# Kernel optimization log

Measured on AMD Instinct MI355X. Metric: run time of the kernel, lower is better.

The kernel has to match this reference:

```python
import jax, jax.numpy as jnp
import numpy as np

D_MODEL = 512
D_INNER = 1024   # expand=2
D_STATE = 16
D_CONV = 4
DT_RANK = 32     # ceil(d_model/16)
B, L = 2, 2048


def _params(kbase):
    kk = jax.random.split(kbase, 9)
    n = lambda k, s, sc: jax.random.normal(k, s, jnp.float32) * sc
    return dict(
        Win=n(kk[0], (2 * D_INNER, D_MODEL), D_MODEL ** -0.5),
        convw=n(kk[1], (D_INNER, 1, D_CONV), 0.2),
        convb=n(kk[2], (D_INNER,), 0.02),
        Wx=n(kk[3], (DT_RANK + 2 * D_STATE, D_INNER), D_INNER ** -0.5),
        Wdt=n(kk[4], (D_INNER, DT_RANK), DT_RANK ** -0.5),
        dtb=n(kk[5], (D_INNER,), 0.1),
        Alog=n(kk[6], (D_INNER, D_STATE), 0.5),
        Dp=n(kk[7], (D_INNER,), 1.0),
        Wout=n(kk[8], (D_MODEL, D_INNER), D_INNER ** -0.5),
    )


def setup_inputs() -> dict:
    key = jax.random.key(0)
    k0, kf, kr = jax.random.split(key, 3)
    inp = {"hidden_states": jax.random.normal(k0, (B, L, D_MODEL), jnp.float32)}
    for name, v in _params(kf).items():
        inp[name + "_f"] = v
    for name, v in _params(kr).items():
        inp[name + "_r"] = v
    return inp


def _mamba(x, Win, convw, convb, Wx, Wdt, dtb, Alog, Dp, Wout):
    # x: (B, L, D_MODEL)
    Bb = x.shape[0]
    xz = jnp.einsum('bld,ed->ble', x, Win)            # (B, L, 2*D_INNER)
    xs, z = jnp.split(xz, 2, axis=-1)
    # causal depthwise conv over length
    xc = jnp.swapaxes(xs, 1, 2)                       # (B, D_INNER, L)
    xc = jax.lax.conv_general_dilated(
        xc, convw, (1,), [(D_CONV - 1, 0)], feature_group_count=D_INNER)
    xs = jax.nn.silu(jnp.swapaxes(xc + convb[None, :, None], 1, 2))  # (B, L, D_INNER)
    # input-dependent SSM params
    x_dbl = jnp.einsum('bld,ed->ble', xs, Wx)         # (B, L, DT_RANK+2*D_STATE)
    dt = x_dbl[..., :DT_RANK]
    Bm = x_dbl[..., DT_RANK:DT_RANK + D_STATE]        # (B, L, D_STATE)
    Cm = x_dbl[..., DT_RANK + D_STATE:]               # (B, L, D_STATE)
    dt = jax.nn.softplus(jnp.einsum('blr,dr->bld', dt, Wdt) + dtb)   # (B, L, D_INNER)
    A = -jnp.exp(Alog)                                # (D_INNER, D_STATE), strictly negative
    dA = jnp.exp(dt[..., None] * A)                   # (B, L, D_INNER, D_STATE)
    dBu = dt[..., None] * Bm[:, :, None, :] * xs[..., None]

    def step(h, inp):
        dA_t, dBu_t, C_t = inp
        h = dA_t * h + dBu_t                          # (B, D_INNER, D_STATE)
        return h, jnp.einsum('bds,bs->bd', h, C_t)

    h0 = jnp.zeros((Bb, D_INNER, D_STATE), x.dtype)
    _, ys = jax.lax.scan(
        step, h0,
        (jnp.moveaxis(dA, 1, 0), jnp.moveaxis(dBu, 1, 0), jnp.moveaxis(Cm, 1, 0)))
    y = jnp.moveaxis(ys, 0, 1) + xs * Dp              # (B, L, D_INNER)
    y = y * jax.nn.silu(z)                            # gated output
    return jnp.einsum('bld,ed->ble', y, Wout)         # (B, L, D_MODEL)


def reference(hidden_states,
              Win_f, convw_f, convb_f, Wx_f, Wdt_f, dtb_f, Alog_f, Dp_f, Wout_f,
              Win_r, convw_r, convb_r, Wx_r, Wdt_r, dtb_r, Alog_r, Dp_r, Wout_r):
    out_f = _mamba(hidden_states, Win_f, convw_f, convb_f, Wx_f, Wdt_f, dtb_f,
                   Alog_f, Dp_f, Wout_f)
    out_r = _mamba(hidden_states[:, ::-1, :], Win_r, convw_r, convb_r, Wx_r,
                   Wdt_r, dtb_r, Alog_r, Dp_r, Wout_r)[:, ::-1, :]
    return out_f + out_r  # bidirectional_strategy == 'add'
```

## Files before the change

kernel.cpp:

```cpp
#include <hip/hip_runtime.h>
#include <cmath>

#define B_   2
#define L_   2048
#define DM_  512
#define DI_  1024
#define DS_  16
#define DTR_ 32
#define M_   (B_*L_)
#define NC_  64
#define CL_  32
#define KS_  8
#define LOG2E_ 1.44269504088896340736f
#define LN2_   0.69314718055994530942f

typedef __attribute__((ext_vector_type(8))) short short8;
typedef __attribute__((ext_vector_type(4))) float floatx4;

__device__ inline unsigned short f2bf(float f) {
  unsigned u = __float_as_uint(f);
  unsigned r = (u + 0x7fffu + ((u >> 16) & 1u)) >> 16;
  return (unsigned short)r;
}
__device__ inline float bf2f(unsigned short u) {
  return __uint_as_float(((unsigned)u) << 16);
}
__device__ inline unsigned short f2h(float f) {
  _Float16 h = (_Float16)f;
  return *(unsigned short*)&h;
}
__device__ inline float h2f(unsigned short u) {
  _Float16 h = *(_Float16*)&u;
  return (float)h;
}
__device__ inline float fexp2(float x) { return __builtin_amdgcn_exp2f(x); }
__device__ inline float flog2(float x) { return __builtin_amdgcn_logf(x); }

__device__ inline void gload_lds16(const unsigned short* g, unsigned short* l) {
  __builtin_amdgcn_global_load_lds(
      (const __attribute__((address_space(1))) void*)g,
      (__attribute__((address_space(3))) void*)l, 16, 0, 0);
}

__global__ __launch_bounds__(256, 2) void gemm1_mfma_k(
    const unsigned short* __restrict__ A,
    const unsigned short* __restrict__ Wf, const unsigned short* __restrict__ Wr,
    unsigned short* __restrict__ Cf, unsigned short* __restrict__ Cr,
    int N, int K)
{
  __shared__ unsigned short At[2][128 * 32];
  __shared__ unsigned short Wtf[2][128 * 32];
  __shared__ unsigned short Wtr[2][128 * 32];
  const int tid  = threadIdx.x;
  const int w    = tid >> 6;
  const int lane = tid & 63;
  const int wm   = w >> 1, wn = w & 1;
  const int row0 = blockIdx.y * 128, col0 = blockIdx.x * 128;
  const int lrow  = lane >> 2;
  const int lkoff = (lane & 3) * 8;
  const int fr = lane & 15;
  const int fq = (lane >> 4) * 8;

  floatx4 accf[4][4], accr[4][4];
#pragma unroll
  for (int i = 0; i < 4; ++i)
#pragma unroll
    for (int j = 0; j < 4; ++j)
#pragma unroll
      for (int r = 0; r < 4; ++r) { accf[i][j][r] = 0.f; accr[i][j][r] = 0.f; }

  auto stage = [&](int buf, int k0) {
#pragma unroll
    for (int j = 0; j < 2; ++j) {
      int r = w * 32 + j * 16;
      gload_lds16(A  + (size_t)(row0 + r + lrow) * K + k0 + lkoff, At[buf]  + r * 32);
      gload_lds16(Wf + (size_t)(col0 + r + lrow) * K + k0 + lkoff, Wtf[buf] + r * 32);
      gload_lds16(Wr + (size_t)(col0 + r + lrow) * K + k0 + lkoff, Wtr[buf] + r * 32);
    }
  };
  auto compute = [&](int buf) {
    short8 af[4], bff[4], bfr[4];
#pragma unroll
    for (int i = 0; i < 4; ++i) {
      af[i]  = *(const short8*)&At[buf][(64 * wm + 16 * i + fr) * 32 + fq];
      bff[i] = *(const short8*)&Wtf[buf][(64 * wn + 16 * i + fr) * 32 + fq];
      bfr[i] = *(const short8*)&Wtr[buf][(64 * wn + 16 * i + fr) * 32 + fq];
    }
#pragma unroll
    for (int i = 0; i < 4; ++i)
#pragma unroll
      for (int j = 0; j < 4; ++j) {
        accf[i][j] = __builtin_amdgcn_mfma_f32_16x16x32_bf16(af[i], bff[j], accf[i][j], 0, 0, 0);
        accr[i][j] = __builtin_amdgcn_mfma_f32_16x16x32_bf16(af[i], bfr[j], accr[i][j], 0, 0, 0);
      }
  };

  const int NT = K >> 5;
  stage(0, 0);
  __syncthreads();
  int cur = 0;
  for (int t = 0; t < NT - 1; ++t) {
    stage(cur ^ 1, (t + 1) << 5);
    compute(cur);
    __syncthreads();
    cur ^= 1;
  }
  compute(cur);

#pragma unroll
  for (int i = 0; i < 4; ++i) {
    int rg = row0 + 64 * wm + 16 * i + ((lane >> 4) << 2);
#pragma unroll
    for (int j = 0; j < 4; ++j) {
      int cg = col0 + 64 * wn + 16 * j + (lane & 15);
#pragma unroll
      for (int r = 0; r < 4; ++r) {
        Cf[(size_t)(rg + r) * N + cg] = f2bf(accf[i][j][r]);
        Cr[(size_t)(rg + r) * N + cg] = f2bf(accr[i][j][r]);
      }
    }
  }
}

__global__ __launch_bounds__(256) void gemm4_fused_k(
    const unsigned short* __restrict__ ybf, const unsigned short* __restrict__ Woutbf,
    const unsigned short* __restrict__ ybr, const unsigned short* __restrict__ Woutbr,
    float* __restrict__ out)
{
  __shared__ unsigned short At[2][2][64 * 32];
  __shared__ unsigned short Wt[2][2][64 * 32];
  const int tid  = threadIdx.x;
  const int w    = tid >> 6;
  const int lane = tid & 63;
  const int col0 = blockIdx.x * 64;
  const int row0 = blockIdx.y * 64;
  const int lrow  = lane >> 2;
  const int lkoff = (lane & 3) * 8;
  const int fr = lane & 15;
  const int fq = (lane >> 4) * 8;

  floatx4 acc[4];
#pragma unroll
  for (int j = 0; j < 4; ++j)
#pragma unroll
    for (int r = 0; r < 4; ++r) acc[j][r] = 0.f;

  auto stage = [&](int buf, int t) {
    const unsigned short* A = (t & 16) ? ybr : ybf;
    const unsigned short* W = (t & 16) ? Woutbr : Woutbf;
    const int k0 = (t & 15) << 6;
#pragma unroll
    for (int h = 0; h < 2; ++h) {
      gload_lds16(A + (size_t)(row0 + 16 * w + lrow) * DI_ + k0 + 32 * h + lkoff,
                  At[buf][h] + (16 * w) * 32);
      gload_lds16(W + (size_t)(col0 + 16 * w + lrow) * DI_ + k0 + 32 * h + lkoff,
                  Wt[buf][h] + (16 * w) * 32);
    }
  };
  auto compute = [&](int buf) {
    short8 af[2], bf[2][4];
#pragma unroll
    for (int h = 0; h < 2; ++h) {
      af[h] = *(const short8*)&At[buf][h][(16 * w + fr) * 32 + fq];
#pragma unroll
      for (int j = 0; j < 4; ++j)
        bf[h][j] = *(const short8*)&Wt[buf][h][(16 * j + fr) * 32 + fq];
    }
#pragma unroll
    for (int h = 0; h < 2; ++h)
#pragma unroll
      for (int j = 0; j < 4; ++j)
        acc[j] = __builtin_amdgcn_mfma_f32_16x16x32_bf16(af[h], bf[h][j], acc[j], 0, 0, 0);
  };

  stage(0, 0);
  __syncthreads();
  int cur = 0;
  for (int t = 0; t < 31; ++t) {
    stage(cur ^ 1, t + 1);
    compute(cur);
    __syncthreads();
    cur ^= 1;
  }
  compute(cur);

  const int rg = row0 + 16 * w + ((lane >> 4) << 2);
#pragma unroll
  for (int j = 0; j < 4; ++j) {
    int cg = col0 + 16 * j + (lane & 15);
#pragma unroll
    for (int r = 0; r < 4; ++r)
      out[(size_t)(rg + r) * DM_ + cg] = acc[j][r];
  }
}

__global__ __launch_bounds__(256) void gemm2_mfma_k(
    const unsigned short* __restrict__ xsbf, const unsigned short* __restrict__ xsbr,
    const unsigned short* __restrict__ Wxbf, const unsigned short* __restrict__ Wxbr,
    float* __restrict__ part)
{
  __shared__ unsigned short At[2][128 * 32];
  __shared__ unsigned short Wt[2][64 * 32];
  const int tid  = threadIdx.x;
  const int w    = tid >> 6;
  const int lane = tid & 63;
  const int ks   = blockIdx.x;
  const int row0 = blockIdx.y * 128;
  const int dir  = blockIdx.z;
  const unsigned short* A = dir ? xsbr : xsbf;
  const unsigned short* W = dir ? Wxbr : Wxbf;
  const int kbase = ks * (DI_ / KS_);
  const int lrow  = lane >> 2;
  const int lkoff = (lane & 3) * 8;
  const int fr = lane & 15;
  const int fq = (lane >> 4) * 8;

  floatx4 acc[2][4];
#pragma unroll
  for (int i = 0; i < 2; ++i)
#pragma unroll
    for (int j = 0; j < 4; ++j)
#pragma unroll
      for (int r = 0; r < 4; ++r) acc[i][j][r] = 0.f;

  auto stage = [&](int buf, int k0) {
#pragma unroll
    for (int j = 0; j < 2; ++j) {
      int r = w * 32 + j * 16;
      gload_lds16(A + (size_t)(row0 + r + lrow) * DI_ + kbase + k0 + lkoff, At[buf] + r * 32);
    }
    int r = w * 16;
    gload_lds16(W + (size_t)(r + lrow) * DI_ + kbase + k0 + lkoff, Wt[buf] + r * 32);
  };
  auto compute = [&](int buf) {
    short8 af[2], bf[4];
#pragma unroll
    for (int i = 0; i < 2; ++i)
      af[i] = *(const short8*)&At[buf][(32 * w + 16 * i + fr) * 32 + fq];
#pragma unroll
    for (int j = 0; j < 4; ++j)
      bf[j] = *(const short8*)&Wt[buf][(16 * j + fr) * 32 + fq];
#pragma unroll
    for (int i = 0; i < 2; ++i)
#pragma unroll
      for (int j = 0; j < 4; ++j)
        acc[i][j] = __builtin_amdgcn_mfma_f32_16x16x32_bf16(af[i], bf[j], acc[i][j], 0, 0, 0);
  };

  const int NT = (DI_ / KS_) >> 5;
  stage(0, 0);
  __syncthreads();
  int cur = 0;
  for (int t = 0; t < NT - 1; ++t) {
    stage(cur ^ 1, (t + 1) << 5);
    compute(cur);
    __syncthreads();
    cur ^= 1;
  }
  compute(cur);

  float* dst = part + (((size_t)dir * KS_ + ks) * M_) * 64;
#pragma unroll
  for (int i = 0; i < 2; ++i) {
    int rg = row0 + 32 * w + 16 * i + ((lane >> 4) << 2);
#pragma unroll
    for (int j = 0; j < 4; ++j) {
      int cg = 16 * j + (lane & 15);
#pragma unroll
      for (int r = 0; r < 4; ++r)
        dst[(size_t)(rg + r) * 64 + cg] = acc[i][j][r];
    }
  }
}

__global__ __launch_bounds__(256) void reduce_part_k(
    const float* __restrict__ part, float* __restrict__ xdf, float* __restrict__ xdr,
    unsigned short* __restrict__ drbf, unsigned short* __restrict__ drbr)
{
  int g = blockIdx.x * 256 + threadIdx.x;
  int n4  = g & 15;
  int m   = (g >> 4) & (M_ - 1);
  int dir = g >> 16;
  const float* p = part + ((size_t)dir * KS_ * M_ + m) * 64 + n4 * 4;
  float4 s = make_float4(0.f, 0.f, 0.f, 0.f);
#pragma unroll
  for (int ks = 0; ks < KS_; ++ks) {
    float4 v = *(const float4*)(p + (size_t)ks * M_ * 64);
    s.x += v.x; s.y += v.y; s.z += v.z; s.w += v.w;
  }
  float* xd = dir ? xdr : xdf;
  *(float4*)(xd + (size_t)m * 64 + n4 * 4) = s;
  if (n4 < 8) {
    unsigned short* dr = dir ? drbr : drbf;
    ushort4 o;
    o.x = f2bf(s.x); o.y = f2bf(s.y); o.z = f2bf(s.z); o.w = f2bf(s.w);
    *(ushort4*)(dr + (size_t)m * 32 + n4 * 4) = o;
  }
}

struct CastArgs {
  const float* src[9];
  unsigned short* dst[9];
  int start[9];
  int n[9];
};

__global__ __launch_bounds__(256) void cast_multi_k(
    CastArgs a, int total4,
    const float* __restrict__ Alf, const float* __restrict__ Alr,
    float* __restrict__ Atf, float* __restrict__ Atr)
{
  int g = blockIdx.x * 256 + threadIdx.x;
  if (g >= total4) return;
  if (g < 8192) {
    const float* Al = (g < 4096) ? Alf : Alr;
    float* At = (g < 4096) ? Atf : Atr;
    int off = (g & 4095) * 4;
    float4 v = *(const float4*)(Al + off);
    float4 o = make_float4(-__expf(v.x) * LOG2E_, -__expf(v.y) * LOG2E_,
                           -__expf(v.z) * LOG2E_, -__expf(v.w) * LOG2E_);
    *(float4*)(At + off) = o;
  }
  int e = g * 4;
#pragma unroll 1
  for (int s = 0; s < 9; ++s) {
    if (e < a.start[s] + a.n[s]) {
      int off = e - a.start[s];
      float4 v = *(const float4*)(a.src[s] + off);
      ushort4 o;
      o.x = f2bf(v.x); o.y = f2bf(v.y); o.z = f2bf(v.z); o.w = f2bf(v.w);
      *(ushort4*)(a.dst[s] + off) = o;
      return;
    }
  }
}

__global__ __launch_bounds__(256) void gemm3_mfma_k(
    const unsigned short* __restrict__ drbf, const unsigned short* __restrict__ drbr,
    const unsigned short* __restrict__ Wdtbf, const unsigned short* __restrict__ Wdtbr,
    const float* __restrict__ b0, const float* __restrict__ b1,
    unsigned short* __restrict__ C0, unsigned short* __restrict__ C1)
{
  __shared__ unsigned short At[128 * 32];
  __shared__ unsigned short Wt[128 * 32];
  const unsigned short* A = blockIdx.z ? drbr : drbf;
  const unsigned short* W = blockIdx.z ? Wdtbr : Wdtbf;
  const float* bias = blockIdx.z ? b1 : b0;
  unsigned short* C = blockIdx.z ? C1 : C0;
  const int tid  = threadIdx.x;
  const int w    = tid >> 6;
  const int lane = tid & 63;
  const int wm   = w >> 1, wn = w & 1;
  const int row0 = blockIdx.y * 128, col0 = blockIdx.x * 128;
  const int lrow  = lane >> 2;
  const int lkoff = (lane & 3) * 8;
  const int fr = lane & 15;
  const int fq = (lane >> 4) * 8;

#pragma unroll
  for (int j = 0; j < 2; ++j) {
    int r = w * 32 + j * 16;
    gload_lds16(A + (size_t)(row0 + r + lrow) * DTR_ + lkoff, At + r * 32);
    gload_lds16(W + (size_t)(col0 + r + lrow) * DTR_ + lkoff, Wt + r * 32);
  }
  __syncthreads();
  short8 af[4], bf[4];
#pragma unroll
  for (int i = 0; i < 4; ++i) {
    af[i] = *(const short8*)&At[(64 * wm + 16 * i + fr) * 32 + fq];
    bf[i] = *(const short8*)&Wt[(64 * wn + 16 * i + fr) * 32 + fq];
  }
  floatx4 acc[4][4];
#pragma unroll
  for (int i = 0; i < 4; ++i)
#pragma unroll
    for (int j = 0; j < 4; ++j) {
#pragma unroll
      for (int r = 0; r < 4; ++r) acc[i][j][r] = 0.f;
      acc[i][j] = __builtin_amdgcn_mfma_f32_16x16x32_bf16(af[i], bf[j], acc[i][j], 0, 0, 0);
    }
#pragma unroll
  for (int i = 0; i < 4; ++i) {
    int rg = row0 + 64 * wm + 16 * i + ((lane >> 4) << 2);
#pragma unroll
    for (int j = 0; j < 4; ++j) {
      int cg = col0 + 64 * wn + 16 * j + (lane & 15);
      float bv = bias[cg];
#pragma unroll
      for (int r = 0; r < 4; ++r) {
        float v = acc[i][j][r] + bv;
        float e = fexp2(-fabsf(v) * LOG2E_);
        float sp = fmaxf(v, 0.f) + LN2_ * flog2(1.f + e);
        C[(size_t)(rg + r) * DI_ + cg] = f2h(sp);
      }
    }
  }
}

__global__ __launch_bounds__(256) void conv_silu_k(
    const unsigned short* __restrict__ xzbf, const unsigned short* __restrict__ xzbr,
    const float* __restrict__ cwf, const float* __restrict__ cbf,
    const float* __restrict__ cwr, const float* __restrict__ cbr,
    unsigned short* __restrict__ xsbf, unsigned short* __restrict__ xsbr)
{
  int bid = blockIdx.x;
  int t2  = bid & (L_ / 2 - 1);
  int b   = (bid >> 10) & (B_ - 1);
  int dir = bid >> 11;
  int t   = t2 << 1;
  const unsigned short* xz = dir ? xzbr : xzbf;
  const float* cw = dir ? cwr : cwf;
  const float* cb = dir ? cbr : cbf;
  unsigned short* xsb = dir ? xsbr : xsbf;
  int d0 = threadIdx.x << 2;
  float wv[4][4];
#pragma unroll
  for (int i = 0; i < 4; ++i) {
    float4 w4 = *(const float4*)(cw + (size_t)(d0 + i) * 4);
    wv[i][0] = w4.x; wv[i][1] = w4.y; wv[i][2] = w4.z; wv[i][3] = w4.w;
  }
  float4 cbv = *(const float4*)(cb + d0);
  float accA[4] = {cbv.x, cbv.y, cbv.z, cbv.w};
  float accB[4] = {cbv.x, cbv.y, cbv.z, cbv.w};
#pragma unroll
  for (int j = 0; j < 5; ++j) {
    int tt = dir ? (t + 4 - j) : (t - 3 + j);
    if (tt >= 0 && tt < L_) {
      ushort4 v = *(const ushort4*)(xz + ((size_t)b * L_ + tt) * 2048 + d0);
      float f0 = bf2f(v.x), f1 = bf2f(v.y), f2 = bf2f(v.z), f3 = bf2f(v.w);
      if (j < 4) {
        accA[0] = fmaf(wv[0][j], f0, accA[0]);
        accA[1] = fmaf(wv[1][j], f1, accA[1]);
        accA[2] = fmaf(wv[2][j], f2, accA[2]);
        accA[3] = fmaf(wv[3][j], f3, accA[3]);
      }
      if (j >= 1) {
        accB[0] = fmaf(wv[0][j - 1], f0, accB[0]);
        accB[1] = fmaf(wv[1][j - 1], f1, accB[1]);
        accB[2] = fmaf(wv[2][j - 1], f2, accB[2]);
        accB[3] = fmaf(wv[3][j - 1], f3, accB[3]);
      }
    }
  }
  int tA = dir ? t + 1 : t;
  int tB = dir ? t : t + 1;
  ushort4 oa, ob;
#pragma unroll
  for (int i = 0; i < 4; ++i) {
    float sa = accA[i] * __builtin_amdgcn_rcpf(1.f + fexp2(-accA[i] * LOG2E_));
    float sb = accB[i] * __builtin_amdgcn_rcpf(1.f + fexp2(-accB[i] * LOG2E_));
    ((unsigned short*)&oa)[i] = f2bf(sa);
    ((unsigned short*)&ob)[i] = f2bf(sb);
  }
  *(ushort4*)(xsb + ((size_t)b * L_ + tA) * DI_ + d0) = oa;
  *(ushort4*)(xsb + ((size_t)b * L_ + tB) * DI_ + d0) = ob;
}

__global__ __launch_bounds__(256) void scan_passA_k(
    const unsigned short* __restrict__ dtf, const unsigned short* __restrict__ dtr,
    const unsigned short* __restrict__ xsbf, const unsigned short* __restrict__ xsbr,
    const float* __restrict__ xdf, const float* __restrict__ xdr,
    const float* __restrict__ Atabf, const float* __restrict__ Atabr,
    float* __restrict__ E, float* __restrict__ dts)
{
  __shared__ float bS[CL_][16];
  int bid  = blockIdx.x;
  int dgrp = bid & 3;
  int c    = (bid >> 2) & (NC_ - 1);
  int b    = (bid >> 8) & 1;
  int dir  = bid >> 9;
  int d    = (dgrp << 8) + threadIdx.x;
  const unsigned short* dt = dir ? dtr : dtf;
  const unsigned short* xs = dir ? xsbr : xsbf;
  const float* xd = dir ? xdr : xdf;
  const float* At = dir ? Atabr : Atabf;
  if (threadIdx.x < CL_ * 4) {
    int li = threadIdx.x >> 2;
    int lc = threadIdx.x & 3;
    *(float4*)&bS[li][lc * 4] =
        *(const float4*)(xd + ((size_t)b * L_ + c * CL_ + li) * 64 + 32 + lc * 4);
  }
  float Ai2[16];
#pragma unroll
  for (int q = 0; q < 4; ++q) {
    float4 a4 = *(const float4*)(At + (size_t)d * 16 + q * 4);
    Ai2[4*q] = a4.x; Ai2[4*q+1] = a4.y; Ai2[4*q+2] = a4.z; Ai2[4*q+3] = a4.w;
  }
  float h[16];
#pragma unroll
  for (int s = 0; s < 16; ++s) h[s] = 0.f;
  int t0 = c * CL_ + (dir ? CL_ - 1 : 0);
  const long sdt = (dir ? -1L : 1L) * DI_;
  const unsigned short* dtp = dt + ((size_t)b * L_ + t0) * DI_ + d;
  const unsigned short* xsp = xs + ((size_t)b * L_ + t0) * DI_ + d;
  float dtsum = 0.f;
  __syncthreads();
#pragma unroll 2
  for (int i = 0; i < CL_; ++i) {
    int row = dir ? (CL_ - 1 - i) : i;
    float dtv = h2f(*dtp);
    float xv  = bf2f(*xsp);
    float Bv[16];
#pragma unroll
    for (int q = 0; q < 4; ++q) {
      float4 bq = *(const float4*)&bS[row][4 * q];
      Bv[4*q] = bq.x; Bv[4*q+1] = bq.y; Bv[4*q+2] = bq.z; Bv[4*q+3] = bq.w;
    }
    float dtx = dtv * xv;
    dtsum += dtv;
#pragma unroll
    for (int s = 0; s < 16; ++s) {
      float dA = fexp2(dtv * Ai2[s]);
      h[s] = fmaf(dA, h[s], dtx * Bv[s]);
    }
    dtp += sdt; xsp += sdt;
  }
  size_t base = ((((size_t)dir * B_ + b) * NC_ + c) * DI_ + d) * 16;
#pragma unroll
  for (int q = 0; q < 4; ++q)
    *(float4*)(E + base + q * 4) = make_float4(h[4*q], h[4*q+1], h[4*q+2], h[4*q+3]);
  dts[(((size_t)dir * B_ + b) * NC_ + c) * DI_ + d] = dtsum;
}

__global__ __launch_bounds__(256) void scan_prefix_k(
    const float* __restrict__ E, const float* __restrict__ dts,
    const float* __restrict__ Atabf, const float* __restrict__ Atabr,
    float* __restrict__ Hin)
{
  int gid = blockIdx.x * 256 + threadIdx.x;
  int s   = gid & 15;
  int d   = (gid >> 4) & (DI_ - 1);
  int b   = (gid >> 14) & 1;
  int dir = gid >> 15;
  float Ai2 = (dir ? Atabr : Atabf)[(size_t)d * 16 + s];
  size_t eb  = (((size_t)dir * B_ + b) * NC_) * DI_ * 16 + (size_t)d * 16 + s;
  size_t db2 = (((size_t)dir * B_ + b) * NC_) * DI_ + d;
  const long es = (long)DI_ * 16;
  float h = 0.f;
  if (!dir) {
    size_t idx = eb;
    size_t di  = db2;
    float Ec = E[idx], dc = dts[di];
#pragma unroll 2
    for (int c = 0; c < NC_ - 1; ++c) {
      float En = E[idx + es];
      float dn = dts[di + DI_];
      Hin[idx] = h;
      h = fmaf(fexp2(dc * Ai2), h, Ec);
      Ec = En; dc = dn; idx += es; di += DI_;
    }
    Hin[idx] = h;
  } else {
    size_t idx = eb + (size_t)(NC_ - 1) * es;
    size_t di  = db2 + (size_t)(NC_ - 1) * DI_;
    float Ec = E[idx], dc = dts[di];
#pragma unroll 2
    for (int c = 0; c < NC_ - 1; ++c) {
      float En = E[idx - es];
      float dn = dts[di - DI_];
      Hin[idx] = h;
      h = fmaf(fexp2(dc * Ai2), h, Ec);
      Ec = En; dc = dn; idx -= es; di -= DI_;
    }
    Hin[idx] = h;
  }
}

__global__ __launch_bounds__(256) void scan_passC_k(
    const unsigned short* __restrict__ dtf, const unsigned short* __restrict__ dtr,
    const unsigned short* __restrict__ xsbf, const unsigned short* __restrict__ xsbr,
    const float* __restrict__ xdf, const float* __restrict__ xdr,
    const unsigned short* __restrict__ xzbf, const unsigned short* __restrict__ xzbr,
    const float* __restrict__ Atabf, const float* __restrict__ Atabr,
    const float* __restrict__ Dpf, const float* __restrict__ Dpr,
    const float* __restrict__ Hin,
    unsigned short* __restrict__ ybf, unsigned short* __restrict__ ybr)
{
  __shared__ float bcS[CL_][32];
  int bid  = blockIdx.x;
  int dgrp = bid & 3;
  int c    = (bid >> 2) & (NC_ - 1);
  int b    = (bid >> 8) & 1;
  int dir  = bid >> 9;
  int d    = (dgrp << 8) + threadIdx.x;
  const unsigned short* dt  = dir ? dtr : dtf;
  const unsigned short* xs = dir ? xsbr : xsbf;
  const float* xd  = dir ? xdr : xdf;
  const unsigned short* xz = dir ? xzbr : xzbf;
  const float* At  = dir ? Atabr : Atabf;
  unsigned short* yb = dir ? ybr : ybf;
  float Dpv = (dir ? Dpr : Dpf)[d];
  {
    int li = threadIdx.x >> 3;
    int lc = threadIdx.x & 7;
    *(float4*)&bcS[li][lc * 4] =
        *(const float4*)(xd + ((size_t)b * L_ + c * CL_ + li) * 64 + 32 + lc * 4);
  }
  float Ai2[16];
#pragma unroll
  for (int q = 0; q < 4; ++q) {
    float4 a4 = *(const float4*)(At + (size_t)d * 16 + q * 4);
    Ai2[4*q] = a4.x; Ai2[4*q+1] = a4.y; Ai2[4*q+2] = a4.z; Ai2[4*q+3] = a4.w;
  }
  size_t hb = ((((size_t)dir * B_ + b) * NC_ + c) * DI_ + d) * 16;
  float h[16];
#pragma unroll
  for (int q = 0; q < 4; ++q) {
    float4 hv = *(const float4*)(Hin + hb + q * 4);
    h[4*q] = hv.x; h[4*q+1] = hv.y; h[4*q+2] = hv.z; h[4*q+3] = hv.w;
  }
  int t0 = c * CL_ + (dir ? CL_ - 1 : 0);
  const long sdt = (dir ? -1L : 1L) * DI_;
  const long sz_ = (dir ? -1L : 1L) * 2048;
  const unsigned short* dtp = dt + ((size_t)b * L_ + t0) * DI_ + d;
  const unsigned short* xsp = xs + ((size_t)b * L_ + t0) * DI_ + d;
  const unsigned short* zp = xz + ((size_t)b * L_ + t0) * 2048 + DI_ + d;
  unsigned short* ybp = yb + ((size_t)b * L_ + t0) * DI_ + d;
  __syncthreads();
#pragma unroll 2
  for (int i = 0; i < CL_; ++i) {
    int row = dir ? (CL_ - 1 - i) : i;
    float dtv = h2f(*dtp);
    float xv  = bf2f(*xsp);
    float z   = bf2f(*zp);
    float Bv[16], Cv[16];
#pragma unroll
    for (int q = 0; q < 4; ++q) {
      float4 bq = *(const float4*)&bcS[row][4 * q];
      float4 cq = *(const float4*)&bcS[row][16 + 4 * q];
      Bv[4*q] = bq.x; Bv[4*q+1] = bq.y; Bv[4*q+2] = bq.z; Bv[4*q+3] = bq.w;
      Cv[4*q] = cq.x; Cv[4*q+1] = cq.y; Cv[4*q+2] = cq.z; Cv[4*q+3] = cq.w;
    }
    float dtx = dtv * xv;
    float yacc = 0.f;
#pragma unroll
    for (int s = 0; s < 16; ++s) {
      float dA = fexp2(dtv * Ai2[s]);
      h[s] = fmaf(dA, h[s], dtx * Bv[s]);
      yacc = fmaf(h[s], Cv[s], yacc);
    }
    float yv = fmaf(xv, Dpv, yacc);
    float sz = z * __builtin_amdgcn_rcpf(1.f + fexp2(-z * LOG2E_));
    *ybp = f2bf(yv * sz);
    dtp += sdt; xsp += sdt; zp += sz_; ybp += sdt;
  }
}

extern "C" void kernel_launch(void* const* d_in, const int* in_sizes, int n_in,
                              void* d_out, int out_size, void* d_ws, size_t ws_size,
                              hipStream_t stream)
{
  const float* x       = (const float*)d_in[0];
  const float* Win_f   = (const float*)d_in[1];
  const float* convw_f = (const float*)d_in[2];
  const float* convb_f = (const float*)d_in[3];
  const float* Wx_f    = (const float*)d_in[4];
  const float* Wdt_f   = (const float*)d_in[5];
  const float* dtb_f   = (const float*)d_in[6];
  const float* Alog_f  = (const float*)d_in[7];
  const float* Dp_f    = (const float*)d_in[8];
  const float* Wout_f  = (const float*)d_in[9];
  const float* Win_r   = (const float*)d_in[10];
  const float* convw_r = (const float*)d_in[11];
  const float* convb_r = (const float*)d_in[12];
  const float* Wx_r    = (const float*)d_in[13];
  const float* Wdt_r   = (const float*)d_in[14];
  const float* dtb_r   = (const float*)d_in[15];
  const float* Alog_r  = (const float*)d_in[16];
  const float* Dp_r    = (const float*)d_in[17];
  const float* Wout_r  = (const float*)d_in[18];
  float* out = (float*)d_out;

  float* ws  = (float*)d_ws;
  float* xdf = ws;
  float* xdr = xdf + (size_t)M_ * 64;
  unsigned short* dtf = (unsigned short*)(xdr + (size_t)M_ * 64);
  unsigned short* dtr = dtf + (size_t)M_ * DI_;
  float* Eb  = (float*)(dtr + (size_t)M_ * DI_);
  float* Hb  = Eb + (size_t)2 * B_ * NC_ * DI_ * 16;
  float* dtsb = Hb + (size_t)2 * B_ * NC_ * DI_ * 16;
  float* part2 = Eb;
  unsigned short* xzbf    = (unsigned short*)(dtsb + (size_t)2 * B_ * NC_ * DI_);
  unsigned short* xzbr    = xzbf + (size_t)M_ * 2048;
  unsigned short* xb      = xzbr + (size_t)M_ * 2048;
  unsigned short* Winb_f  = xb + (size_t)M_ * DM_;
  unsigned short* Winb_r  = Winb_f + (size_t)2048 * DM_;
  unsigned short* Woutb_f = Winb_r + (size_t)2048 * DM_;
  unsigned short* Woutb_r = Woutb_f + (size_t)DM_ * DI_;
  unsigned short* ybf     = Woutb_r + (size_t)DM_ * DI_;
  unsigned short* ybr     = ybf + (size_t)M_ * DI_;
  unsigned short* xsbf    = ybr + (size_t)M_ * DI_;
  unsigned short* xsbr    = xsbf + (size_t)M_ * DI_;
  unsigned short* Wxb_f   = xsbr + (size_t)M_ * DI_;
  unsigned short* Wxb_r   = Wxb_f + (size_t)64 * DI_;
  unsigned short* Wdtb_f  = Wxb_r + (size_t)64 * DI_;
  unsigned short* Wdtb_r  = Wdtb_f + (size_t)DI_ * DTR_;
  unsigned short* drbf    = Wdtb_r + (size_t)DI_ * DTR_;
  unsigned short* drbr    = drbf + (size_t)M_ * DTR_;
  float* Atabf = (float*)(drbr + (size_t)M_ * DTR_);
  float* Atabr = Atabf + (size_t)DI_ * DS_;

  dim3 blk(256);

  {
    CastArgs ca;
    ca.src[0] = x;      ca.dst[0] = xb;      ca.n[0] = M_ * DM_;
    ca.src[1] = Win_f;  ca.dst[1] = Winb_f;  ca.n[1] = 2048 * DM_;
    ca.src[2] = Win_r;  ca.dst[2] = Winb_r;  ca.n[2] = 2048 * DM_;
    ca.src[3] = Wout_f; ca.dst[3] = Woutb_f; ca.n[3] = DM_ * DI_;
    ca.src[4] = Wout_r; ca.dst[4] = Woutb_r; ca.n[4] = DM_ * DI_;
    ca.src[5] = Wx_f;   ca.dst[5] = Wxb_f;   ca.n[5] = 64 * DI_;
    ca.src[6] = Wx_r;   ca.dst[6] = Wxb_r;   ca.n[6] = 64 * DI_;
    ca.src[7] = Wdt_f;  ca.dst[7] = Wdtb_f;  ca.n[7] = DI_ * DTR_;
    ca.src[8] = Wdt_r;  ca.dst[8] = Wdtb_r;  ca.n[8] = DI_ * DTR_;
    int st = 0;
    for (int s = 0; s < 9; ++s) { ca.start[s] = st; st += ca.n[s]; }
    int total4 = st / 4;
    cast_multi_k<<<(total4 + 255) / 256, blk, 0, stream>>>(
        ca, total4, Alog_f, Alog_r, Atabf, Atabr);
  }

  gemm1_mfma_k<<<dim3(2048 / 128, M_ / 128), blk, 0, stream>>>(
      xb, Winb_f, Winb_r, xzbf, xzbr, 2048, DM_);

  conv_silu_k<<<2 * B_ * (L_ / 2), blk, 0, stream>>>(xzbf, xzbr, convw_f, convb_f,
      convw_r, convb_r, xsbf, xsbr);

  gemm2_mfma_k<<<dim3(KS_, M_ / 128, 2), blk, 0, stream>>>(
      xsbf, xsbr, Wxb_f, Wxb_r, part2);
  reduce_part_k<<<(2 * M_ * 16) / 256, blk, 0, stream>>>(part2, xdf, xdr,
      drbf, drbr);

  gemm3_mfma_k<<<dim3(DI_ / 128, M_ / 128, 2), blk, 0, stream>>>(
      drbf, drbr, Wdtb_f, Wdtb_r, dtb_f, dtb_r, dtf, dtr);

  scan_passA_k<<<2 * B_ * NC_ * 4, blk, 0, stream>>>(dtf, dtr, xsbf, xsbr,
      xdf, xdr, Atabf, Atabr, Eb, dtsb);
  scan_prefix_k<<<(2 * B_ * DI_ * 16) / 256, blk, 0, stream>>>(
      Eb, dtsb, Atabf, Atabr, Hb);
  scan_passC_k<<<2 * B_ * NC_ * 4, blk, 0, stream>>>(dtf, dtr, xsbf, xsbr,
      xdf, xdr, xzbf, xzbr, Atabf, Atabr, Dp_f, Dp_r, Hb, ybf, ybr);

  gemm4_fused_k<<<dim3(DM_ / 64, M_ / 64), blk, 0, stream>>>(
      ybf, Woutb_f, ybr, Woutb_r, out);
}
```

Measured before the change: 261.0 us.

## Store chunk scan states in fp16, batch prefix loads, widen conv outputs per block

The chunk-end states E and the chunk-entry states Hin move from fp32 to fp16 storage, which halves the traffic between pass A, the prefix scan and pass C. The prefix scan now preloads eight chunks of E and dts before running the serial recurrence, so more loads are in flight. The conv+SiLU kernel computes four timesteps per thread instead of two, reusing the overlapping input rows and launching half as many blocks. The cost is fp16 rounding of the carried scan states, which could lose precision or overflow if states grow large.

```diff
diff --git a/kernel.cpp b/kernel.cpp
--- a/kernel.cpp
+++ b/kernel.cpp
@@ -404,10 +404,10 @@
     unsigned short* __restrict__ xsbf, unsigned short* __restrict__ xsbr)
 {
   int bid = blockIdx.x;
-  int t2  = bid & (L_ / 2 - 1);
-  int b   = (bid >> 10) & (B_ - 1);
-  int dir = bid >> 11;
-  int t   = t2 << 1;
+  int tg  = bid & (L_ / 4 - 1);
+  int b   = (bid >> 9) & (B_ - 1);
+  int dir = bid >> 10;
+  int t   = tg << 2;
   const unsigned short* xz = dir ? xzbr : xzbf;
   const float* cw = dir ? cwr : cwf;
   const float* cb = dir ? cbr : cbf;
@@ -420,40 +420,39 @@
     wv[i][0] = w4.x; wv[i][1] = w4.y; wv[i][2] = w4.z; wv[i][3] = w4.w;
   }
   float4 cbv = *(const float4*)(cb + d0);
-  float accA[4] = {cbv.x, cbv.y, cbv.z, cbv.w};
-  float accB[4] = {cbv.x, cbv.y, cbv.z, cbv.w};
-#pragma unroll
-  for (int j = 0; j < 5; ++j) {
-    int tt = dir ? (t + 4 - j) : (t - 3 + j);
+  float acc[4][4];
+#pragma unroll
+  for (int k = 0; k < 4; ++k) {
+    acc[k][0] = cbv.x; acc[k][1] = cbv.y; acc[k][2] = cbv.z; acc[k][3] = cbv.w;
+  }
+#pragma unroll
+  for (int m = 0; m < 7; ++m) {
+    int tt = dir ? (t + 6 - m) : (t - 3 + m);
     if (tt >= 0 && tt < L_) {
       ushort4 v = *(const ushort4*)(xz + ((size_t)b * L_ + tt) * 2048 + d0);
       float f0 = bf2f(v.x), f1 = bf2f(v.y), f2 = bf2f(v.z), f3 = bf2f(v.w);
-      if (j < 4) {
-        accA[0] = fmaf(wv[0][j], f0, accA[0]);
-        accA[1] = fmaf(wv[1][j], f1, accA[1]);
-        accA[2] = fmaf(wv[2][j], f2, accA[2]);
-        accA[3] = fmaf(wv[3][j], f3, accA[3]);
+#pragma unroll
+      for (int k = 0; k < 4; ++k) {
+        int j = dir ? (m - 3 + k) : (m - k);
+        if (j >= 0 && j < 4) {
+          acc[k][0] = fmaf(wv[0][j], f0, acc[k][0]);
+          acc[k][1] = fmaf(wv[1][j], f1, acc[k][1]);
+          acc[k][2] = fmaf(wv[2][j], f2, acc[k][2]);
+          acc[k][3] = fmaf(wv[3][j], f3, acc[k][3]);
+        }
       }
-      if (j >= 1) {
-        accB[0] = fmaf(wv[0][j - 1], f0, accB[0]);
-        accB[1] = fmaf(wv[1][j - 1], f1, accB[1]);
-        accB[2] = fmaf(wv[2][j - 1], f2, accB[2]);
-        accB[3] = fmaf(wv[3][j - 1], f3, accB[3]);
-      }
-    }
-  }
-  int tA = dir ? t + 1 : t;
-  int tB = dir ? t : t + 1;
-  ushort4 oa, ob;
-#pragma unroll
-  for (int i = 0; i < 4; ++i) {
-    float sa = accA[i] * __builtin_amdgcn_rcpf(1.f + fexp2(-accA[i] * LOG2E_));
-    float sb = accB[i] * __builtin_amdgcn_rcpf(1.f + fexp2(-accB[i] * LOG2E_));
-    ((unsigned short*)&oa)[i] = f2bf(sa);
-    ((unsigned short*)&ob)[i] = f2bf(sb);
-  }
-  *(ushort4*)(xsb + ((size_t)b * L_ + tA) * DI_ + d0) = oa;
-  *(ushort4*)(xsb + ((size_t)b * L_ + tB) * DI_ + d0) = ob;
+    }
+  }
+#pragma unroll
+  for (int k = 0; k < 4; ++k) {
+    ushort4 o;
+#pragma unroll
+    for (int i = 0; i < 4; ++i) {
+      float s = acc[k][i] * __builtin_amdgcn_rcpf(1.f + fexp2(-acc[k][i] * LOG2E_));
+      ((unsigned short*)&o)[i] = f2bf(s);
+    }
+    *(ushort4*)(xsb + ((size_t)b * L_ + (t + k)) * DI_ + d0) = o;
+  }
 }
 
 __global__ __launch_bounds__(256) void scan_passA_k(
@@ -461,7 +460,7 @@
     const unsigned short* __restrict__ xsbf, const unsigned short* __restrict__ xsbr,
     const float* __restrict__ xdf, const float* __restrict__ xdr,
     const float* __restrict__ Atabf, const float* __restrict__ Atabr,
-    float* __restrict__ E, float* __restrict__ dts)
+    unsigned short* __restrict__ E, float* __restrict__ dts)
 {
   __shared__ float bS[CL_][16];
   int bid  = blockIdx.x;
@@ -516,16 +515,19 @@
     dtp += sdt; xsp += sdt;
   }
   size_t base = ((((size_t)dir * B_ + b) * NC_ + c) * DI_ + d) * 16;
-#pragma unroll
-  for (int q = 0; q < 4; ++q)
-    *(float4*)(E + base + q * 4) = make_float4(h[4*q], h[4*q+1], h[4*q+2], h[4*q+3]);
+  unsigned pk[8];
+#pragma unroll
+  for (int q = 0; q < 8; ++q)
+    pk[q] = (unsigned)f2h(h[2*q]) | ((unsigned)f2h(h[2*q+1]) << 16);
+  *(uint4*)(E + base)     = make_uint4(pk[0], pk[1], pk[2], pk[3]);
+  *(uint4*)(E + base + 8) = make_uint4(pk[4], pk[5], pk[6], pk[7]);
   dts[(((size_t)dir * B_ + b) * NC_ + c) * DI_ + d] = dtsum;
 }
 
 __global__ __launch_bounds__(256) void scan_prefix_k(
-    const float* __restrict__ E, const float* __restrict__ dts,
+    const unsigned short* __restrict__ E, const float* __restrict__ dts,
     const float* __restrict__ Atabf, const float* __restrict__ Atabr,
-    float* __restrict__ Hin)
+    unsigned short* __restrict__ Hin)
 {
   int gid = blockIdx.x * 256 + threadIdx.x;
   int s   = gid & 15;
@@ -535,34 +537,44 @@
   float Ai2 = (dir ? Atabr : Atabf)[(size_t)d * 16 + s];
   size_t eb  = (((size_t)dir * B_ + b) * NC_) * DI_ * 16 + (size_t)d * 16 + s;
   size_t db2 = (((size_t)dir * B_ + b) * NC_) * DI_ + d;
-  const long es = (long)DI_ * 16;
+  const size_t es = (size_t)DI_ * 16;
   float h = 0.f;
   if (!dir) {
     size_t idx = eb;
     size_t di  = db2;
-    float Ec = E[idx], dc = dts[di];
-#pragma unroll 2
-    for (int c = 0; c < NC_ - 1; ++c) {
-      float En = E[idx + es];
-      float dn = dts[di + DI_];
-      Hin[idx] = h;
-      h = fmaf(fexp2(dc * Ai2), h, Ec);
-      Ec = En; dc = dn; idx += es; di += DI_;
-    }
-    Hin[idx] = h;
+#pragma unroll 1
+    for (int cb = 0; cb < NC_; cb += 8) {
+      unsigned short Ev[8]; float dv[8];
+#pragma unroll
+      for (int k = 0; k < 8; ++k) {
+        Ev[k] = E[idx + (size_t)k * es];
+        dv[k] = dts[di + (size_t)k * DI_];
+      }
+#pragma unroll
+      for (int k = 0; k < 8; ++k) {
+        Hin[idx + (size_t)k * es] = f2h(h);
+        h = fmaf(fexp2(dv[k] * Ai2), h, h2f(Ev[k]));
+      }
+      idx += 8 * es; di += 8 * (size_t)DI_;
+    }
   } else {
     size_t idx = eb + (size_t)(NC_ - 1) * es;
     size_t di  = db2 + (size_t)(NC_ - 1) * DI_;
-    float Ec = E[idx], dc = dts[di];
-#pragma unroll 2
-    for (int c = 0; c < NC_ - 1; ++c) {
-      float En = E[idx - es];
-      float dn = dts[di - DI_];
-      Hin[idx] = h;
-      h = fmaf(fexp2(dc * Ai2), h, Ec);
-      Ec = En; dc = dn; idx -= es; di -= DI_;
-    }
-    Hin[idx] = h;
+#pragma unroll 1
+    for (int cb = 0; cb < NC_; cb += 8) {
+      unsigned short Ev[8]; float dv[8];
+#pragma unroll
+      for (int k = 0; k < 8; ++k) {
+        Ev[k] = E[idx - (size_t)k * es];
+        dv[k] = dts[di - (size_t)k * DI_];
+      }
+#pragma unroll
+      for (int k = 0; k < 8; ++k) {
+        Hin[idx - (size_t)k * es] = f2h(h);
+        h = fmaf(fexp2(dv[k] * Ai2), h, h2f(Ev[k]));
+      }
+      idx -= 8 * es; di -= 8 * (size_t)DI_;
+    }
   }
 }
 
@@ -573,7 +585,7 @@
     const unsigned short* __restrict__ xzbf, const unsigned short* __restrict__ xzbr,
     const float* __restrict__ Atabf, const float* __restrict__ Atabr,
     const float* __restrict__ Dpf, const float* __restrict__ Dpr,
-    const float* __restrict__ Hin,
+    const unsigned short* __restrict__ Hin,
     unsigned short* __restrict__ ybf, unsigned short* __restrict__ ybr)
 {
   __shared__ float bcS[CL_][32];
@@ -604,10 +616,15 @@
   }
   size_t hb = ((((size_t)dir * B_ + b) * NC_ + c) * DI_ + d) * 16;
   float h[16];
-#pragma unroll
-  for (int q = 0; q < 4; ++q) {
-    float4 hv = *(const float4*)(Hin + hb + q * 4);
-    h[4*q] = hv.x; h[4*q+1] = hv.y; h[4*q+2] = hv.z; h[4*q+3] = hv.w;
+  {
+    uint4 ha = *(const uint4*)(Hin + hb);
+    uint4 hbv = *(const uint4*)(Hin + hb + 8);
+    unsigned hw[8] = {ha.x, ha.y, ha.z, ha.w, hbv.x, hbv.y, hbv.z, hbv.w};
+#pragma unroll
+    for (int q = 0; q < 8; ++q) {
+      h[2*q]   = h2f((unsigned short)(hw[q] & 0xffffu));
+      h[2*q+1] = h2f((unsigned short)(hw[q] >> 16));
+    }
   }
   int t0 = c * CL_ + (dir ? CL_ - 1 : 0);
   const long sdt = (dir ? -1L : 1L) * DI_;
@@ -676,10 +693,10 @@
   float* xdr = xdf + (size_t)M_ * 64;
   unsigned short* dtf = (unsigned short*)(xdr + (size_t)M_ * 64);
   unsigned short* dtr = dtf + (size_t)M_ * DI_;
-  float* Eb  = (float*)(dtr + (size_t)M_ * DI_);
-  float* Hb  = Eb + (size_t)2 * B_ * NC_ * DI_ * 16;
-  float* dtsb = Hb + (size_t)2 * B_ * NC_ * DI_ * 16;
-  float* part2 = Eb;
+  unsigned short* Eh = dtr + (size_t)M_ * DI_;
+  unsigned short* Hh = Eh + (size_t)2 * B_ * NC_ * DI_ * 16;
+  float* dtsb = (float*)(Hh + (size_t)2 * B_ * NC_ * DI_ * 16);
+  float* part2 = (float*)Eh;
   unsigned short* xzbf    = (unsigned short*)(dtsb + (size_t)2 * B_ * NC_ * DI_);
   unsigned short* xzbr    = xzbf + (size_t)M_ * 2048;
   unsigned short* xb      = xzbr + (size_t)M_ * 2048;
@@ -723,7 +740,7 @@
   gemm1_mfma_k<<<dim3(2048 / 128, M_ / 128), blk, 0, stream>>>(
       xb, Winb_f, Winb_r, xzbf, xzbr, 2048, DM_);
 
-  conv_silu_k<<<2 * B_ * (L_ / 2), blk, 0, stream>>>(xzbf, xzbr, convw_f, convb_f,
+  conv_silu_k<<<2 * B_ * (L_ / 4), blk, 0, stream>>>(xzbf, xzbr, convw_f, convb_f,
       convw_r, convb_r, xsbf, xsbr);
 
   gemm2_mfma_k<<<dim3(KS_, M_ / 128, 2), blk, 0, stream>>>(
@@ -735,11 +752,11 @@
       drbf, drbr, Wdtb_f, Wdtb_r, dtb_f, dtb_r, dtf, dtr);
 
   scan_passA_k<<<2 * B_ * NC_ * 4, blk, 0, stream>>>(dtf, dtr, xsbf, xsbr,
-      xdf, xdr, Atabf, Atabr, Eb, dtsb);
+      xdf, xdr, Atabf, Atabr, Eh, dtsb);
   scan_prefix_k<<<(2 * B_ * DI_ * 16) / 256, blk, 0, stream>>>(
-      Eb, dtsb, Atabf, Atabr, Hb);
+      Eh, dtsb, Atabf, Atabr, Hh);
   scan_passC_k<<<2 * B_ * NC_ * 4, blk, 0, stream>>>(dtf, dtr, xsbf, xsbr,
-      xdf, xdr, xzbf, xzbr, Atabf, Atabr, Dp_f, Dp_r, Hb, ybf, ybr);
+      xdf, xdr, xzbf, xzbr, Atabf, Atabr, Dp_f, Dp_r, Hh, ybf, ybr);
 
   gemm4_fused_k<<<dim3(DM_ / 64, M_ / 64), blk, 0, stream>>>(
       ybf, Woutb_f, ybr, Woutb_r, out);
```

Result: faster. 249.3 us (-4.5%).
